# Performance work log

Measured on AMD Instinct MI355X. Metric: run time of the kernel, lower is better.

Reference implementation:

```python
import jax, jax.numpy as jnp
import numpy as np

N = 65536      # nodes
E = 262144     # edges per metapath
K = 8          # sampled edges per node
NMP = 2        # metapaths (n_mp)
DEPTH = 2      # layers
H = 4          # heads
D = 256        # prep_len / hidden (= H*PH)
PH = 64        # per-head output dim
ED = 64        # raw edge embedding dim


def setup_inputs() -> dict:
    key = jax.random.key(0)
    ks = jax.random.split(key, 16)
    s = 1.0 / np.sqrt(D)
    return {
        "feats": jax.random.normal(ks[0], (N, D), jnp.float32),
        "edge_emb": jax.random.normal(ks[1], (NMP, E, ED), jnp.float32),
        "edge_node_adj": jax.random.randint(ks[2], (NMP, E, 2), 0, N, dtype=jnp.int32),
        "node2edge_idx": jax.random.randint(ks[3], (NMP, N, K), 0, E, dtype=jnp.int32),
        "W_prep0": jax.random.normal(ks[4], (D, D), jnp.float32) * s,
        "W_prep1": jax.random.normal(ks[5], (D, D), jnp.float32) * s,
        "W_eprep": jax.random.normal(ks[6], (NMP, ED, D), jnp.float32) * (1.0 / np.sqrt(ED)),
        "a_e": jax.random.normal(ks[7], (NMP, DEPTH, H, D), jnp.float32) * s,
        "a_n": jax.random.normal(ks[8], (NMP, DEPTH, H, D), jnp.float32) * s,
        "W_e": jax.random.normal(ks[9], (NMP, DEPTH, H, D, PH), jnp.float32) * s,
        "a_s": jax.random.normal(ks[10], (NMP, DEPTH, H, D), jnp.float32) * s,
        "a_edge": jax.random.normal(ks[11], (NMP, DEPTH, H, D), jnp.float32) * s,
        "W_self": jax.random.normal(ks[12], (NMP, DEPTH, H, D, PH), jnp.float32) * s,
        "W_nb": jax.random.normal(ks[13], (NMP, DEPTH, H, D, PH), jnp.float32) * s,
    }


def _forward(feats, edge_emb, edge_node_adj, node2edge_idx,
             W_prep0, W_prep1, W_eprep, a_e, a_n, W_e, a_s, a_edge, W_self, W_nb):
    dummy = feats @ W_prep0     # prep(layer_idx=0)  [N,D]
    base = feats @ W_prep1      # prep(layer_idx=1)  [N,D]
    outputs = []
    for mp in range(NMP):
        x = base
        edges = edge_emb[mp] @ W_eprep[mp]           # [E,D]
        ena = edge_node_adj[mp]                      # [E,2]
        n2e = node2edge_idx[mp]                      # [N,K]
        skips = []
        for L in range(DEPTH):
            # --- edge aggregator: gather 2 endpoint node feats, attend, project ---
            ep = x[ena]                              # [E,2,D] gather
            s_e = jax.nn.leaky_relu(
                jnp.einsum('eqd,hd->ehq', ep, a_n[mp, L])
                + jnp.einsum('ed,hd->eh', edges, a_e[mp, L])[..., None], 0.2)  # [E,H,2]
            alp = jax.nn.softmax(s_e, axis=-1)
            agg = jnp.einsum('ehq,eqd->ehd', alp, ep)                          # [E,H,D]
            e_out = jax.nn.elu(
                jnp.einsum('ehd,hdp->ehp', edges[:, None, :] + agg, W_e[mp, L])
            ).reshape(E, H * PH)                                               # [E,D]
            # --- node aggregator: gather K sampled edge feats (OLD edges), attend ---
            xin = x if L > 0 else dummy              # layer 0 self-feature uses dummy prep
            eg = edges[n2e]                          # [N,K,D] gather
            s_n = jax.nn.leaky_relu(
                jnp.einsum('nd,hd->nh', xin, a_s[mp, L])[:, :, None]
                + jnp.einsum('nkd,hd->nhk', eg, a_edge[mp, L]), 0.2)           # [N,H,K]
            aln = jax.nn.softmax(s_n, axis=-1)
            nag = jnp.einsum('nhk,nkd->nhd', aln, eg)                          # [N,H,D]
            n_out = jax.nn.elu(
                jnp.einsum('nd,hdp->nhp', xin, W_self[mp, L])
                + jnp.einsum('nhd,hdp->nhp', nag, W_nb[mp, L])
            ).reshape(N, H * PH)                                               # [N,D]
            skips.append(n_out)
            x = n_out
            edges = e_out
        outputs.append(jnp.concatenate(skips, axis=-1))   # [N, DEPTH*D]
    return jnp.stack(outputs, axis=0)                     # [NMP, N, DEPTH*D]


def reference(feats, edge_emb, edge_node_adj, node2edge_idx,
              W_prep0, W_prep1, W_eprep, a_e, a_n, W_e, a_s, a_edge, W_self, W_nb):
    return _forward(feats, edge_emb, edge_node_adj, node2edge_idx,
                    W_prep0, W_prep1, W_eprep, a_e, a_n, W_e, a_s, a_edge, W_self, W_nb)
```

## Files before the change

kernel.cpp:

```cpp
#include <hip/hip_runtime.h>

typedef unsigned short ushort_t;
typedef unsigned int uint_t;

#define N_NODES 65536
#define N_EDGES 262144

typedef __attribute__((ext_vector_type(8))) short bf16x8;
typedef __attribute__((ext_vector_type(4))) float f32x4;

__device__ __forceinline__ ushort_t f2b(float x) {
  uint_t u = __float_as_uint(x);
  u += 0x7fffu + ((u >> 16) & 1u);
  return (ushort_t)(u >> 16);
}
__device__ __forceinline__ void dec8(uint4 v, float* f) {
  f[0] = __uint_as_float(v.x << 16); f[1] = __uint_as_float(v.x & 0xffff0000u);
  f[2] = __uint_as_float(v.y << 16); f[3] = __uint_as_float(v.y & 0xffff0000u);
  f[4] = __uint_as_float(v.z << 16); f[5] = __uint_as_float(v.z & 0xffff0000u);
  f[6] = __uint_as_float(v.w << 16); f[7] = __uint_as_float(v.w & 0xffff0000u);
}
__device__ __forceinline__ void dec4(uint2 v, float* f) {
  f[0] = __uint_as_float(v.x << 16); f[1] = __uint_as_float(v.x & 0xffff0000u);
  f[2] = __uint_as_float(v.y << 16); f[3] = __uint_as_float(v.y & 0xffff0000u);
}
__device__ __forceinline__ uint4 enc8(const float* f) {
  uint4 v;
  v.x = (uint_t)f2b(f[0]) | ((uint_t)f2b(f[1]) << 16);
  v.y = (uint_t)f2b(f[2]) | ((uint_t)f2b(f[3]) << 16);
  v.z = (uint_t)f2b(f[4]) | ((uint_t)f2b(f[5]) << 16);
  v.w = (uint_t)f2b(f[6]) | ((uint_t)f2b(f[7]) << 16);
  return v;
}
__device__ __forceinline__ uint2 enc4(const float* f) {
  uint2 v;
  v.x = (uint_t)f2b(f[0]) | ((uint_t)f2b(f[1]) << 16);
  v.y = (uint_t)f2b(f[2]) | ((uint_t)f2b(f[3]) << 16);
  return v;
}
__device__ __forceinline__ void ld8(const float* p, float* f) {
  float4 v0 = *(const float4*)p;
  float4 v1 = *(const float4*)(p + 4);
  f[0]=v0.x; f[1]=v0.y; f[2]=v0.z; f[3]=v0.w;
  f[4]=v1.x; f[5]=v1.y; f[6]=v1.z; f[7]=v1.w;
}

#define ELUF(v) ((v) > 0.f ? (v) : __expf(v) - 1.f)

__device__ __forceinline__ void async16(void* lds, const void* g) {
  __builtin_amdgcn_global_load_lds(
      (const __attribute__((address_space(1))) void*)g,
      (__attribute__((address_space(3))) void*)lds, 16, 0, 0);
}

__global__ void wt_kernel(const float* __restrict__ src, ushort_t* __restrict__ dst,
                          int K, int N) {
  long m = blockIdx.y;
  long base = m * (long)K * N;
  int tid = blockIdx.x * 256 + threadIdx.x;
  if (tid >= K * N) return;
  int k = tid % K, n = tid / K;
  dst[base + (long)n * K + k] = f2b(src[base + (long)k * N + n]);
}

__global__ __launch_bounds__(256, 2) void gemm_mfma(
    const float* __restrict__ A, const ushort_t* __restrict__ Wt,
    ushort_t* __restrict__ outb, int K) {
  __shared__ __align__(16) char smem[4096 + 16384];
  ushort_t (*sA)[32] = (ushort_t(*)[32])smem;
  ushort_t (*sB)[32] = (ushort_t(*)[32])(smem + 4096);
  int t = threadIdx.x, w = t >> 6, l = t & 63;
  long r0 = (long)blockIdx.x * 64;
  f32x4 zero = {0.f, 0.f, 0.f, 0.f};
  f32x4 acc[4][4];
#pragma unroll
  for (int mt = 0; mt < 4; ++mt)
#pragma unroll
    for (int nt = 0; nt < 4; ++nt) acc[mt][nt] = zero;

  for (int kc = 0; kc < K / 32; ++kc) {
    __syncthreads();
    {
      int r = t >> 2, ks8 = (t & 3) * 8;
      float f[8]; ld8(A + (r0 + r) * (long)K + kc * 32 + ks8, f);
      *(uint4*)&sA[r][ks8] = enc8(f);
    }
#pragma unroll
    for (int j = 0; j < 4; ++j) {
      int u = (w * 4 + j) * 64 + l;
      int n = u >> 2, ks = u & 3;
      async16((char*)sB + (w * 4 + j) * 1024, Wt + (long)n * K + kc * 32 + ks * 8);
    }
    __syncthreads();
    bf16x8 af[4], bf[4];
#pragma unroll
    for (int mt = 0; mt < 4; ++mt)
      af[mt] = *(const bf16x8*)&sA[mt * 16 + (l & 15)][(l >> 4) * 8];
#pragma unroll
    for (int nt = 0; nt < 4; ++nt)
      bf[nt] = *(const bf16x8*)&sB[w * 64 + nt * 16 + (l & 15)][(l >> 4) * 8];
#pragma unroll
    for (int mt = 0; mt < 4; ++mt)
#pragma unroll
      for (int nt = 0; nt < 4; ++nt)
        acc[mt][nt] = __builtin_amdgcn_mfma_f32_16x16x32_bf16(af[mt], bf[nt], acc[mt][nt], 0, 0, 0);
  }
#pragma unroll
  for (int mt = 0; mt < 4; ++mt)
#pragma unroll
    for (int nt = 0; nt < 4; ++nt)
#pragma unroll
      for (int i = 0; i < 4; ++i) {
        long row = r0 + mt * 16 + (l >> 4) * 4 + i;
        int col = w * 64 + nt * 16 + (l & 15);
        outb[row * 256 + col] = f2b(acc[mt][nt][i]);
      }
}

__global__ __launch_bounds__(256, 2) void gemm_eproj(
    const ushort_t* __restrict__ A, const ushort_t* __restrict__ Wt,
    const float* __restrict__ a_edge,
    ushort_t* __restrict__ outb, float* __restrict__ sed) {
  __shared__ __align__(16) char smem[4096 + 16384 + 8192];
  ushort_t (*sA)[32]   = (ushort_t(*)[32])smem;
  ushort_t (*sB)[32]   = (ushort_t(*)[32])(smem + 4096);
  ushort_t (*sAe)[256] = (ushort_t(*)[256])(smem + 20480);
  int t = threadIdx.x, w = t >> 6, l = t & 63;
  long r0 = (long)blockIdx.x * 64;

  {
    int row = t >> 4, seg = (t & 15) * 16;
    float f[16];
    if (row < 4) {
      ld8(a_edge + row * 256 + seg, f);
      ld8(a_edge + row * 256 + seg + 8, f + 8);
    } else {
#pragma unroll
      for (int i = 0; i < 16; ++i) f[i] = 0.f;
    }
    *(uint4*)&sAe[row][seg] = enc8(f);
    *(uint4*)&sAe[row][seg + 8] = enc8(f + 8);
  }

  f32x4 zero = {0.f, 0.f, 0.f, 0.f};
  f32x4 acc[4][4];
  f32x4 accs[4];
#pragma unroll
  for (int mt = 0; mt < 4; ++mt) {
    accs[mt] = zero;
#pragma unroll
    for (int nt = 0; nt < 4; ++nt) acc[mt][nt] = zero;
  }

  for (int kc = 0; kc < 8; ++kc) {
    __syncthreads();
    async16((char*)sA + w * 1024, A + (r0 + (t >> 2)) * 256 + kc * 32 + (t & 3) * 8);
#pragma unroll
    for (int j = 0; j < 4; ++j) {
      int u = (w * 4 + j) * 64 + l;
      int n = u >> 2, ks = u & 3;
      async16((char*)sB + (w * 4 + j) * 1024, Wt + (long)n * 256 + kc * 32 + ks * 8);
    }
    __syncthreads();
    bf16x8 af[4], bf[4];
#pragma unroll
    for (int mt = 0; mt < 4; ++mt)
      af[mt] = *(const bf16x8*)&sA[mt * 16 + (l & 15)][(l >> 4) * 8];
#pragma unroll
    for (int nt = 0; nt < 4; ++nt)
      bf[nt] = *(const bf16x8*)&sB[w * 64 + nt * 16 + (l & 15)][(l >> 4) * 8];
#pragma unroll
    for (int mt = 0; mt < 4; ++mt)
#pragma unroll
      for (int nt = 0; nt < 4; ++nt)
        acc[mt][nt] = __builtin_amdgcn_mfma_f32_16x16x32_bf16(af[mt], bf[nt], acc[mt][nt], 0, 0, 0);
    if (w == 0) {
      bf16x8 bs = *(const bf16x8*)&sAe[l & 15][kc * 32 + (l >> 4) * 8];
#pragma unroll
      for (int mt = 0; mt < 4; ++mt)
        accs[mt] = __builtin_amdgcn_mfma_f32_16x16x32_bf16(af[mt], bs, accs[mt], 0, 0, 0);
    }
  }
#pragma unroll
  for (int mt = 0; mt < 4; ++mt)
#pragma unroll
    for (int nt = 0; nt < 4; ++nt)
#pragma unroll
      for (int i = 0; i < 4; ++i) {
        long row = r0 + mt * 16 + (l >> 4) * 4 + i;
        int col = w * 64 + nt * 16 + (l & 15);
        outb[row * 256 + col] = f2b(acc[mt][nt][i]);
      }
  if (w == 0 && (l & 15) < 4) {
#pragma unroll
    for (int mt = 0; mt < 4; ++mt)
#pragma unroll
      for (int i = 0; i < 4; ++i) {
        long row = r0 + mt * 16 + (l >> 4) * 4 + i;
        sed[row * 4 + (l & 15)] = accs[mt][i];
      }
  }
}

__global__ __launch_bounds__(256, 2) void edge_kernel(
    const ushort_t* __restrict__ xb,
    const ushort_t* __restrict__ ein,
    ushort_t* __restrict__ eout,
    const int* __restrict__ ena,
    const float* __restrict__ a_n, const float* __restrict__ a_e,
    const ushort_t* __restrict__ Wt) {
  __shared__ __align__(16) char smem[8192 + 16384 + 4096 + 1024 + 256 + 16];
  ushort_t (*sY)[32][32] = (ushort_t(*)[32][32])smem;
  ushort_t (*sB)[32]     = (ushort_t(*)[32])(smem + 8192);
  ushort_t (*sAf)[256]   = (ushort_t(*)[256])(smem + 24576);
  float    (*sAlp)[4][2] = (float(*)[4][2])(smem + 28672);
  int* sIdx              = (int*)(smem + 29696);
  ushort_t* sOut         = (ushort_t*)smem;

  int t = threadIdx.x, w = t >> 6, l = t & 63;
  long e0 = (long)blockIdx.x * 32;

  if (t < 64) sIdx[(t & 1) * 32 + (t >> 1)] = ena[(e0 + (t >> 1)) * 2 + (t & 1)];
  {
    int row = t >> 5, dof = (t & 31) * 8;
    const float* src = (row < 4 ? a_n + row * 256 : a_e + (row - 4) * 256) + dof;
    float f[8]; ld8(src, f);
    *(uint4*)&sAf[row][dof] = enc8(f);
  }
  __syncthreads();

  int eT = t >> 3, sT = t & 7;
  int nid0 = sIdx[eT], nid1 = sIdx[32 + eT];
  const ushort_t* pxe = ein + (e0 + eT) * 256;
  const ushort_t* px0 = xb + (long)nid0 * 256;
  const ushort_t* px1 = xb + (long)nid1 * 256;

  float an0[4] = {0,0,0,0}, an1[4] = {0,0,0,0}, aee[4] = {0,0,0,0};
#pragma unroll
  for (int kc = 0; kc < 8; ++kc) {
    int dof = kc * 32 + sT * 4;
    float xe[4], x0[4], x1[4];
    dec4(*(const uint2*)(pxe + dof), xe);
    dec4(*(const uint2*)(px0 + dof), x0);
    dec4(*(const uint2*)(px1 + dof), x1);
#pragma unroll
    for (int h = 0; h < 4; ++h) {
      float av[4], bv[4];
      dec4(*(const uint2*)&sAf[h][dof], av);
      dec4(*(const uint2*)&sAf[4 + h][dof], bv);
#pragma unroll
      for (int d = 0; d < 4; ++d) {
        an0[h] += x0[d] * av[d];
        an1[h] += x1[d] * av[d];
        aee[h] += xe[d] * bv[d];
      }
    }
  }
#pragma unroll
  for (int m = 1; m <= 4; m <<= 1)
#pragma unroll
    for (int h = 0; h < 4; ++h) {
      an0[h] += __shfl_xor(an0[h], m, 64);
      an1[h] += __shfl_xor(an1[h], m, 64);
      aee[h] += __shfl_xor(aee[h], m, 64);
    }
  if (sT == 0) {
#pragma unroll
    for (int h = 0; h < 4; ++h) {
      float s0 = an0[h] + aee[h]; s0 = s0 > 0.f ? s0 : 0.2f * s0;
      float s1 = an1[h] + aee[h]; s1 = s1 > 0.f ? s1 : 0.2f * s1;
      float mx = fmaxf(s0, s1);
      float g0 = __expf(s0 - mx), g1 = __expf(s1 - mx);
      float inv = 1.f / (g0 + g1);
      sAlp[eT][h][0] = g0 * inv;
      sAlp[eT][h][1] = g1 * inv;
    }
  }
  __syncthreads();
  float alp[4][2];
#pragma unroll
  for (int h = 0; h < 4; ++h) {
    alp[h][0] = sAlp[eT][h][0];
    alp[h][1] = sAlp[eT][h][1];
  }

  f32x4 zero = {0.f, 0.f, 0.f, 0.f};
  f32x4 acc[2][4];
#pragma unroll
  for (int mt = 0; mt < 2; ++mt)
#pragma unroll
    for (int nt = 0; nt < 4; ++nt) acc[mt][nt] = zero;

  int ks4 = sT * 4;
  for (int kc = 0; kc < 8; ++kc) {
    __syncthreads();
#pragma unroll
    for (int j = 0; j < 4; ++j) {
      int u = (w * 4 + j) * 64 + l;
      int n = u >> 2, ks = u & 3;
      async16((char*)sB + (w * 4 + j) * 1024, Wt + (long)n * 256 + kc * 32 + ks * 8);
    }
    {
      int dof = kc * 32 + ks4;
      float xe[4], x0[4], x1[4];
      dec4(*(const uint2*)(pxe + dof), xe);
      dec4(*(const uint2*)(px0 + dof), x0);
      dec4(*(const uint2*)(px1 + dof), x1);
#pragma unroll
      for (int h = 0; h < 4; ++h) {
        float y[4];
#pragma unroll
        for (int d = 0; d < 4; ++d)
          y[d] = xe[d] + alp[h][0] * x0[d] + alp[h][1] * x1[d];
        *(uint2*)&sY[h][eT][ks4] = enc4(y);
      }
    }
    __syncthreads();
    bf16x8 af[2], bf[4];
#pragma unroll
    for (int mt = 0; mt < 2; ++mt)
      af[mt] = *(const bf16x8*)&sY[w][mt * 16 + (l & 15)][(l >> 4) * 8];
#pragma unroll
    for (int nt = 0; nt < 4; ++nt)
      bf[nt] = *(const bf16x8*)&sB[w * 64 + nt * 16 + (l & 15)][(l >> 4) * 8];
#pragma unroll
    for (int mt = 0; mt < 2; ++mt)
#pragma unroll
      for (int nt = 0; nt < 4; ++nt)
        acc[mt][nt] = __builtin_amdgcn_mfma_f32_16x16x32_bf16(af[mt], bf[nt], acc[mt][nt], 0, 0, 0);
  }
  __syncthreads();
#pragma unroll
  for (int mt = 0; mt < 2; ++mt)
#pragma unroll
    for (int nt = 0; nt < 4; ++nt)
#pragma unroll
      for (int i = 0; i < 4; ++i) {
        int row = mt * 16 + (l >> 4) * 4 + i;
        int col = w * 64 + nt * 16 + (l & 15);
        sOut[row * 264 + col] = f2b(ELUF(acc[mt][nt][i]));
      }
  __syncthreads();
#pragma unroll
  for (int j = 0; j < 4; ++j) {
    int u = t + j * 256;
    int r = u >> 5, ks = u & 31;
    *(uint4*)(eout + (e0 + r) * 256 + ks * 8) = *(const uint4*)&sOut[r * 264 + ks * 8];
  }
}

__global__ __launch_bounds__(256, 2) void node_out(
    const ushort_t* __restrict__ xb,
    const int* __restrict__ n2e,
    const ushort_t* __restrict__ eproj,
    const float* __restrict__ sed,
    const float* __restrict__ a_s,
    const ushort_t* __restrict__ WtS,
    float* __restrict__ outp,
    ushort_t* __restrict__ xout) {
  __shared__ __align__(16) char smem[33280 + 1024 + 4096 + 4096];
  ushort_t (*sX)[32]   = (ushort_t(*)[32])smem;
  ushort_t (*sBs)[32]  = (ushort_t(*)[32])(smem + 2048);
  ushort_t (*sAs)[256] = (ushort_t(*)[256])(smem + 18432);
  float* sOutF         = (float*)smem;
  int*   sIdx          = (int*)(smem + 33280);
  float* sSe           = (float*)(smem + 34304);
  float* sAln          = (float*)(smem + 38400);
  int t = threadIdx.x, w = t >> 6, l = t & 63;
  long n0 = (long)blockIdx.x * 32;

  {
    int e = n2e[n0 * 8 + t];
    sIdx[t] = e;
    *(float4*)&sSe[t * 4] = *(const float4*)(sed + (long)e * 4);
  }
  if (t < 128) {
    int row = t >> 5, dof = (t & 31) * 8;
    float f[8]; ld8(a_s + row * 256 + dof, f);
    *(uint4*)&sAs[row][dof] = enc8(f);
  }

  f32x4 zero = {0.f, 0.f, 0.f, 0.f};
  f32x4 acc[2][4];
#pragma unroll
  for (int mt = 0; mt < 2; ++mt)
#pragma unroll
    for (int nt = 0; nt < 4; ++nt) acc[mt][nt] = zero;
  float ssp = 0.f;
  int sn = t >> 3, shalf = (t & 1) * 16, sh = (t >> 1) & 3;

  for (int kc = 0; kc < 8; ++kc) {
    __syncthreads();
    if (w == 0) {
#pragma unroll
      for (int j = 0; j < 2; ++j) {
        int u = j * 64 + l;
        int r = u >> 2, ks = u & 3;
        async16((char*)sX + j * 1024, xb + (n0 + r) * 256 + kc * 32 + ks * 8);
      }
    }
#pragma unroll
    for (int j = 0; j < 4; ++j) {
      int u = (w * 4 + j) * 64 + l;
      int n = u >> 2, ks = u & 3;
      async16((char*)sBs + (w * 4 + j) * 1024, WtS + (long)n * 256 + kc * 32 + ks * 8);
    }
    __syncthreads();
    bf16x8 ax[2], bs[4];
#pragma unroll
    for (int mt = 0; mt < 2; ++mt)
      ax[mt] = *(const bf16x8*)&sX[mt * 16 + (l & 15)][(l >> 4) * 8];
#pragma unroll
    for (int nt = 0; nt < 4; ++nt)
      bs[nt] = *(const bf16x8*)&sBs[w * 64 + nt * 16 + (l & 15)][(l >> 4) * 8];
#pragma unroll
    for (int mt = 0; mt < 2; ++mt)
#pragma unroll
      for (int nt = 0; nt < 4; ++nt)
        acc[mt][nt] = __builtin_amdgcn_mfma_f32_16x16x32_bf16(ax[mt], bs[nt], acc[mt][nt], 0, 0, 0);
    {
      float xv[16], av[16];
      dec8(*(const uint4*)&sX[sn][shalf], xv);
      dec8(*(const uint4*)&sX[sn][shalf + 8], xv + 8);
      dec8(*(const uint4*)&sAs[sh][kc * 32 + shalf], av);
      dec8(*(const uint4*)&sAs[sh][kc * 32 + shalf + 8], av + 8);
#pragma unroll
      for (int d = 0; d < 16; ++d) ssp += xv[d] * av[d];
    }
  }
  __syncthreads();
#pragma unroll
  for (int mt = 0; mt < 2; ++mt)
#pragma unroll
    for (int nt = 0; nt < 4; ++nt)
#pragma unroll
      for (int i = 0; i < 4; ++i) {
        int row = mt * 16 + (l >> 4) * 4 + i;
        int col = w * 64 + nt * 16 + (l & 15);
        sOutF[row * 260 + col] = acc[mt][nt][i];
      }
  float ssv = ssp + __shfl_xor(ssp, 1, 64);
  if (!(t & 1)) {
    float sv[8], mx = -1e30f;
#pragma unroll
    for (int k = 0; k < 8; ++k) {
      float s = ssv + sSe[(sn * 8 + k) * 4 + sh];
      s = s > 0.f ? s : 0.2f * s;
      sv[k] = s; mx = fmaxf(mx, s);
    }
    float sum = 0.f;
#pragma unroll
    for (int k = 0; k < 8; ++k) { sv[k] = __expf(sv[k] - mx); sum += sv[k]; }
    float inv = 1.f / sum;
#pragma unroll
    for (int k = 0; k < 8; ++k) sAln[(sn * 4 + sh) * 8 + k] = sv[k] * inv;
  }
  __syncthreads();

  int nT = t >> 3, sT = t & 7, hh = sT >> 1, dof = sT * 32;
  float wts[8];
#pragma unroll
  for (int k = 0; k < 8; ++k) wts[k] = sAln[(nT * 4 + hh) * 8 + k];
  int eidx[8];
#pragma unroll
  for (int k = 0; k < 8; ++k) eidx[k] = sIdx[nT * 8 + k];
  float o[32];
#pragma unroll
  for (int j = 0; j < 8; ++j) {
    float4 sv = *(const float4*)&sOutF[nT * 260 + dof + j * 4];
    o[j * 4 + 0] = sv.x; o[j * 4 + 1] = sv.y; o[j * 4 + 2] = sv.z; o[j * 4 + 3] = sv.w;
  }
#pragma unroll
  for (int k = 0; k < 8; ++k) {
    const ushort_t* pr = eproj + (long)eidx[k] * 256 + dof;
    float v[32];
    dec8(*(const uint4*)(pr),      v);
    dec8(*(const uint4*)(pr + 8),  v + 8);
    dec8(*(const uint4*)(pr + 16), v + 16);
    dec8(*(const uint4*)(pr + 24), v + 24);
    float wk = wts[k];
#pragma unroll
    for (int d = 0; d < 32; ++d) o[d] += wk * v[d];
  }
  long row = n0 + nT;
  float res[32];
#pragma unroll
  for (int d = 0; d < 32; ++d) res[d] = ELUF(o[d]);
  float* po = outp + row * 512 + dof;
#pragma unroll
  for (int j = 0; j < 8; ++j) {
    float4 q;
    q.x = res[j * 4 + 0]; q.y = res[j * 4 + 1]; q.z = res[j * 4 + 2]; q.w = res[j * 4 + 3];
    *(float4*)(po + j * 4) = q;
  }
  if (xout) {
#pragma unroll
    for (int j = 0; j < 4; ++j)
      *(uint4*)(xout + row * 256 + dof + j * 8) = enc8(res + j * 8);
  }
}

extern "C" void kernel_launch(void* const* d_in, const int* in_sizes, int n_in,
                              void* d_out, int out_size, void* d_ws, size_t ws_size,
                              hipStream_t stream) {
  (void)in_sizes; (void)n_in; (void)out_size; (void)ws_size;
  const float* feats  = (const float*)d_in[0];
  const float* eemb   = (const float*)d_in[1];
  const int*   adj    = (const int*)d_in[2];
  const int*   n2e    = (const int*)d_in[3];
  const float* Wp0    = (const float*)d_in[4];
  const float* Wp1    = (const float*)d_in[5];
  const float* Wep    = (const float*)d_in[6];
  const float* a_e    = (const float*)d_in[7];
  const float* a_n    = (const float*)d_in[8];
  const float* W_e    = (const float*)d_in[9];
  const float* a_s    = (const float*)d_in[10];
  const float* a_edge = (const float*)d_in[11];
  const float* W_self = (const float*)d_in[12];
  const float* W_nb   = (const float*)d_in[13];
  float* out = (float*)d_out;

  char* w = (char*)d_ws;
  ushort_t* dummy_bf = (ushort_t*)w; w += (size_t)N_NODES * 256 * 2;
  ushort_t* base_bf  = (ushort_t*)w; w += (size_t)N_NODES * 256 * 2;
  ushort_t* edgesA   = (ushort_t*)w; w += (size_t)N_EDGES * 256 * 2;
  ushort_t* edgesB   = (ushort_t*)w; w += (size_t)N_EDGES * 256 * 2;
  ushort_t* eproj    = (ushort_t*)w; w += (size_t)N_EDGES * 256 * 2;
  float*    sed      = (float*)w;    w += (size_t)N_EDGES * 4 * 4;
  ushort_t* xl1      = (ushort_t*)w; w += (size_t)N_NODES * 256 * 2;
  ushort_t* WtP0     = (ushort_t*)w; w += 256 * 256 * 2;
  ushort_t* WtP1     = (ushort_t*)w; w += 256 * 256 * 2;
  ushort_t* WtEp     = (ushort_t*)w; w += 2 * 256 * 64 * 2;
  ushort_t* WtE      = (ushort_t*)w; w += 16 * 16384 * 2;
  ushort_t* WtS      = (ushort_t*)w; w += 16 * 16384 * 2;
  ushort_t* WtN      = (ushort_t*)w; w += 16 * 16384 * 2;

  wt_kernel<<<dim3(256, 1), 256, 0, stream>>>(Wp0, WtP0, 256, 256);
  wt_kernel<<<dim3(256, 1), 256, 0, stream>>>(Wp1, WtP1, 256, 256);
  wt_kernel<<<dim3(64, 2), 256, 0, stream>>>(Wep, WtEp, 64, 256);
  wt_kernel<<<dim3(64, 16), 256, 0, stream>>>(W_e, WtE, 256, 64);
  wt_kernel<<<dim3(64, 16), 256, 0, stream>>>(W_self, WtS, 256, 64);
  wt_kernel<<<dim3(64, 16), 256, 0, stream>>>(W_nb, WtN, 256, 64);

  gemm_mfma<<<N_NODES / 64, 256, 0, stream>>>(feats, WtP0, dummy_bf, 256);
  gemm_mfma<<<N_NODES / 64, 256, 0, stream>>>(feats, WtP1, base_bf, 256);

  for (int mp = 0; mp < 2; ++mp) {
    const int* adj_mp = adj + (size_t)mp * N_EDGES * 2;
    const int* n2e_mp = n2e + (size_t)mp * N_NODES * 8;
    size_t ao0 = (size_t)(mp * 2 + 0) * 1024, ao1 = (size_t)(mp * 2 + 1) * 1024;
    size_t wo0 = (size_t)(mp * 2 + 0) * 65536, wo1 = (size_t)(mp * 2 + 1) * 65536;

    gemm_mfma<<<N_EDGES / 64, 256, 0, stream>>>(
        eemb + (size_t)mp * N_EDGES * 64, WtEp + (size_t)mp * 16384, edgesA, 64);

    gemm_eproj<<<N_EDGES / 64, 256, 0, stream>>>(edgesA, WtN + wo0, a_edge + ao0, eproj, sed);
    edge_kernel<<<N_EDGES / 32, 256, 0, stream>>>(base_bf, edgesA, edgesB, adj_mp,
                                                  a_n + ao0, a_e + ao0, WtE + wo0);
    node_out<<<N_NODES / 32, 256, 0, stream>>>(dummy_bf, n2e_mp, eproj, sed,
                                               a_s + ao0, WtS + wo0,
                                               out + (size_t)mp * N_NODES * 512, xl1);
    gemm_eproj<<<N_EDGES / 64, 256, 0, stream>>>(edgesB, WtN + wo1, a_edge + ao1, eproj, sed);
    node_out<<<N_NODES / 32, 256, 0, stream>>>(xl1, n2e_mp, eproj, sed,
                                               a_s + ao1, WtS + wo1,
                                               out + (size_t)mp * N_NODES * 512 + 256,
                                               (ushort_t*)nullptr);
  }
}
```

Baseline: 1.589 ms.

## Project edges and nodes through W_e before gather and fuse next-layer projection

The edge aggregator now uses linearity. Edge embeddings and node features are projected through W_e separately, and the per-head attention scores come out of the same MFMA GEMMs. A new edge_combine kernel gathers the projected endpoint rows, mixes them with the attention weights and applies ELU. It then immediately multiplies the result by the next layer's W_nb, so the intermediate edge tensor is never materialized and the separate second gemm_eproj launch disappears. In exchange there is an extra node-sized GEMM, buffers are aliased across stages, and rounding is slightly different because the projection now happens before the mix.

```diff
diff --git a/kernel.cpp b/kernel.cpp
--- a/kernel.cpp
+++ b/kernel.cpp
@@ -119,14 +119,107 @@
 
 __global__ __launch_bounds__(256, 2) void gemm_eproj(
     const ushort_t* __restrict__ A, const ushort_t* __restrict__ Wt,
-    const float* __restrict__ a_edge,
-    ushort_t* __restrict__ outb, float* __restrict__ sed) {
+    const float* __restrict__ a_vec,
+    ushort_t* __restrict__ outb, float* __restrict__ sco) {
   __shared__ __align__(16) char smem[4096 + 16384 + 8192];
   ushort_t (*sA)[32]   = (ushort_t(*)[32])smem;
   ushort_t (*sB)[32]   = (ushort_t(*)[32])(smem + 4096);
   ushort_t (*sAe)[256] = (ushort_t(*)[256])(smem + 20480);
   int t = threadIdx.x, w = t >> 6, l = t & 63;
   long r0 = (long)blockIdx.x * 64;
+
+  {
+    int row = t >> 4, seg = (t & 15) * 16;
+    float f[16];
+    if (row < 4) {
+      ld8(a_vec + row * 256 + seg, f);
+      ld8(a_vec + row * 256 + seg + 8, f + 8);
+    } else {
+#pragma unroll
+      for (int i = 0; i < 16; ++i) f[i] = 0.f;
+    }
+    *(uint4*)&sAe[row][seg] = enc8(f);
+    *(uint4*)&sAe[row][seg + 8] = enc8(f + 8);
+  }
+
+  f32x4 zero = {0.f, 0.f, 0.f, 0.f};
+  f32x4 acc[4][4];
+  f32x4 accs[4];
+#pragma unroll
+  for (int mt = 0; mt < 4; ++mt) {
+    accs[mt] = zero;
+#pragma unroll
+    for (int nt = 0; nt < 4; ++nt) acc[mt][nt] = zero;
+  }
+
+  for (int kc = 0; kc < 8; ++kc) {
+    __syncthreads();
+    async16((char*)sA + w * 1024, A + (r0 + (t >> 2)) * 256 + kc * 32 + (t & 3) * 8);
+#pragma unroll
+    for (int j = 0; j < 4; ++j) {
+      int u = (w * 4 + j) * 64 + l;
+      int n = u >> 2, ks = u & 3;
+      async16((char*)sB + (w * 4 + j) * 1024, Wt + (long)n * 256 + kc * 32 + ks * 8);
+    }
+    __syncthreads();
+    bf16x8 af[4], bf[4];
+#pragma unroll
+    for (int mt = 0; mt < 4; ++mt)
+      af[mt] = *(const bf16x8*)&sA[mt * 16 + (l & 15)][(l >> 4) * 8];
+#pragma unroll
+    for (int nt = 0; nt < 4; ++nt)
+      bf[nt] = *(const bf16x8*)&sB[w * 64 + nt * 16 + (l & 15)][(l >> 4) * 8];
+#pragma unroll
+    for (int mt = 0; mt < 4; ++mt)
+#pragma unroll
+      for (int nt = 0; nt < 4; ++nt)
+        acc[mt][nt] = __builtin_amdgcn_mfma_f32_16x16x32_bf16(af[mt], bf[nt], acc[mt][nt], 0, 0, 0);
+    if (w == 0) {
+      bf16x8 bs = *(const bf16x8*)&sAe[l & 15][kc * 32 + (l >> 4) * 8];
+#pragma unroll
+      for (int mt = 0; mt < 4; ++mt)
+        accs[mt] = __builtin_amdgcn_mfma_f32_16x16x32_bf16(af[mt], bs, accs[mt], 0, 0, 0);
+    }
+  }
+#pragma unroll
+  for (int mt = 0; mt < 4; ++mt)
+#pragma unroll
+    for (int nt = 0; nt < 4; ++nt)
+#pragma unroll
+      for (int i = 0; i < 4; ++i) {
+        long row = r0 + mt * 16 + (l >> 4) * 4 + i;
+        int col = w * 64 + nt * 16 + (l & 15);
+        outb[row * 256 + col] = f2b(acc[mt][nt][i]);
+      }
+  if (w == 0 && (l & 15) < 4) {
+#pragma unroll
+    for (int mt = 0; mt < 4; ++mt)
+#pragma unroll
+      for (int i = 0; i < 4; ++i) {
+        long row = r0 + mt * 16 + (l >> 4) * 4 + i;
+        sco[row * 4 + (l & 15)] = accs[mt][i];
+      }
+  }
+}
+
+__global__ __launch_bounds__(256, 2) void edge_combine(
+    const int* __restrict__ ena,
+    const ushort_t* __restrict__ eprojE,
+    const ushort_t* __restrict__ xprojE,
+    const float* __restrict__ xan,
+    const float* __restrict__ sea,
+    const ushort_t* __restrict__ Wt,
+    const float* __restrict__ a_edge,
+    ushort_t* __restrict__ outb,
+    float* __restrict__ sed) {
+  __shared__ __align__(16) char smem[4096 + 16384 + 8192 + 2048 + 512];
+  ushort_t (*sY)[32]   = (ushort_t(*)[32])smem;
+  ushort_t (*sB)[32]   = (ushort_t(*)[32])(smem + 4096);
+  ushort_t (*sAe)[256] = (ushort_t(*)[256])(smem + 20480);
+  float (*sAlp)[4][2]  = (float(*)[4][2])(smem + 28672);
+  int* sIdx            = (int*)(smem + 30720);
+  int t = threadIdx.x, w = t >> 6, l = t & 63;
+  long e0 = (long)blockIdx.x * 64;
 
   {
     int row = t >> 4, seg = (t & 15) * 16;
@@ -141,6 +234,27 @@
     *(uint4*)&sAe[row][seg] = enc8(f);
     *(uint4*)&sAe[row][seg + 8] = enc8(f + 8);
   }
+  if (t < 128) sIdx[t] = ena[e0 * 2 + t];
+  __syncthreads();
+
+  {
+    int e = t >> 2, h = t & 3;
+    int n0 = sIdx[2 * e], n1 = sIdx[2 * e + 1];
+    float sE = sea[(e0 + e) * 4 + h];
+    float s0 = xan[(long)n0 * 4 + h] + sE; s0 = s0 > 0.f ? s0 : 0.2f * s0;
+    float s1 = xan[(long)n1 * 4 + h] + sE; s1 = s1 > 0.f ? s1 : 0.2f * s1;
+    float mx = fmaxf(s0, s1);
+    float g0 = __expf(s0 - mx), g1 = __expf(s1 - mx);
+    float inv = 1.f / (g0 + g1);
+    sAlp[e][h][0] = g0 * inv;
+    sAlp[e][h][1] = g1 * inv;
+  }
+
+  int r = t >> 2, c0 = (t & 3) * 8;
+  int n0r = sIdx[2 * r], n1r = sIdx[2 * r + 1];
+  const ushort_t* pe = eprojE + (e0 + r) * 256 + c0;
+  const ushort_t* p0 = xprojE + (long)n0r * 256 + c0;
+  const ushort_t* p1 = xprojE + (long)n1r * 256 + c0;
 
   f32x4 zero = {0.f, 0.f, 0.f, 0.f};
   f32x4 acc[4][4];
@@ -154,18 +268,31 @@
 
   for (int kc = 0; kc < 8; ++kc) {
     __syncthreads();
-    async16((char*)sA + w * 1024, A + (r0 + (t >> 2)) * 256 + kc * 32 + (t & 3) * 8);
 #pragma unroll
     for (int j = 0; j < 4; ++j) {
       int u = (w * 4 + j) * 64 + l;
       int n = u >> 2, ks = u & 3;
       async16((char*)sB + (w * 4 + j) * 1024, Wt + (long)n * 256 + kc * 32 + ks * 8);
     }
+    {
+      int h = kc >> 1;
+      float a0 = sAlp[r][h][0], a1 = sAlp[r][h][1];
+      float ep[8], x0[8], x1[8], y[8];
+      dec8(*(const uint4*)(pe + kc * 32), ep);
+      dec8(*(const uint4*)(p0 + kc * 32), x0);
+      dec8(*(const uint4*)(p1 + kc * 32), x1);
+#pragma unroll
+      for (int d = 0; d < 8; ++d) {
+        float v = ep[d] + a0 * x0[d] + a1 * x1[d];
+        y[d] = ELUF(v);
+      }
+      *(uint4*)&sY[r][c0] = enc8(y);
+    }
     __syncthreads();
     bf16x8 af[4], bf[4];
 #pragma unroll
     for (int mt = 0; mt < 4; ++mt)
-      af[mt] = *(const bf16x8*)&sA[mt * 16 + (l & 15)][(l >> 4) * 8];
+      af[mt] = *(const bf16x8*)&sY[mt * 16 + (l & 15)][(l >> 4) * 8];
 #pragma unroll
     for (int nt = 0; nt < 4; ++nt)
       bf[nt] = *(const bf16x8*)&sB[w * 64 + nt * 16 + (l & 15)][(l >> 4) * 8];
@@ -187,7 +314,7 @@
     for (int nt = 0; nt < 4; ++nt)
 #pragma unroll
       for (int i = 0; i < 4; ++i) {
-        long row = r0 + mt * 16 + (l >> 4) * 4 + i;
+        long row = e0 + mt * 16 + (l >> 4) * 4 + i;
         int col = w * 64 + nt * 16 + (l & 15);
         outb[row * 256 + col] = f2b(acc[mt][nt][i]);
       }
@@ -196,156 +323,9 @@
     for (int mt = 0; mt < 4; ++mt)
 #pragma unroll
       for (int i = 0; i < 4; ++i) {
-        long row = r0 + mt * 16 + (l >> 4) * 4 + i;
+        long row = e0 + mt * 16 + (l >> 4) * 4 + i;
         sed[row * 4 + (l & 15)] = accs[mt][i];
       }
-  }
-}
-
-__global__ __launch_bounds__(256, 2) void edge_kernel(
-    const ushort_t* __restrict__ xb,
-    const ushort_t* __restrict__ ein,
-    ushort_t* __restrict__ eout,
-    const int* __restrict__ ena,
-    const float* __restrict__ a_n, const float* __restrict__ a_e,
-    const ushort_t* __restrict__ Wt) {
-  __shared__ __align__(16) char smem[8192 + 16384 + 4096 + 1024 + 256 + 16];
-  ushort_t (*sY)[32][32] = (ushort_t(*)[32][32])smem;
-  ushort_t (*sB)[32]     = (ushort_t(*)[32])(smem + 8192);
-  ushort_t (*sAf)[256]   = (ushort_t(*)[256])(smem + 24576);
-  float    (*sAlp)[4][2] = (float(*)[4][2])(smem + 28672);
-  int* sIdx              = (int*)(smem + 29696);
-  ushort_t* sOut         = (ushort_t*)smem;
-
-  int t = threadIdx.x, w = t >> 6, l = t & 63;
-  long e0 = (long)blockIdx.x * 32;
-
-  if (t < 64) sIdx[(t & 1) * 32 + (t >> 1)] = ena[(e0 + (t >> 1)) * 2 + (t & 1)];
-  {
-    int row = t >> 5, dof = (t & 31) * 8;
-    const float* src = (row < 4 ? a_n + row * 256 : a_e + (row - 4) * 256) + dof;
-    float f[8]; ld8(src, f);
-    *(uint4*)&sAf[row][dof] = enc8(f);
-  }
-  __syncthreads();
-
-  int eT = t >> 3, sT = t & 7;
-  int nid0 = sIdx[eT], nid1 = sIdx[32 + eT];
-  const ushort_t* pxe = ein + (e0 + eT) * 256;
-  const ushort_t* px0 = xb + (long)nid0 * 256;
-  const ushort_t* px1 = xb + (long)nid1 * 256;
-
-  float an0[4] = {0,0,0,0}, an1[4] = {0,0,0,0}, aee[4] = {0,0,0,0};
-#pragma unroll
-  for (int kc = 0; kc < 8; ++kc) {
-    int dof = kc * 32 + sT * 4;
-    float xe[4], x0[4], x1[4];
-    dec4(*(const uint2*)(pxe + dof), xe);
-    dec4(*(const uint2*)(px0 + dof), x0);
-    dec4(*(const uint2*)(px1 + dof), x1);
-#pragma unroll
-    for (int h = 0; h < 4; ++h) {
-      float av[4], bv[4];
-      dec4(*(const uint2*)&sAf[h][dof], av);
-      dec4(*(const uint2*)&sAf[4 + h][dof], bv);
-#pragma unroll
-      for (int d = 0; d < 4; ++d) {
-        an0[h] += x0[d] * av[d];
-        an1[h] += x1[d] * av[d];
-        aee[h] += xe[d] * bv[d];
-      }
-    }
-  }
-#pragma unroll
-  for (int m = 1; m <= 4; m <<= 1)
-#pragma unroll
-    for (int h = 0; h < 4; ++h) {
-      an0[h] += __shfl_xor(an0[h], m, 64);
-      an1[h] += __shfl_xor(an1[h], m, 64);
-      aee[h] += __shfl_xor(aee[h], m, 64);
-    }
-  if (sT == 0) {
-#pragma unroll
-    for (int h = 0; h < 4; ++h) {
-      float s0 = an0[h] + aee[h]; s0 = s0 > 0.f ? s0 : 0.2f * s0;
-      float s1 = an1[h] + aee[h]; s1 = s1 > 0.f ? s1 : 0.2f * s1;
-      float mx = fmaxf(s0, s1);
-      float g0 = __expf(s0 - mx), g1 = __expf(s1 - mx);
-      float inv = 1.f / (g0 + g1);
-      sAlp[eT][h][0] = g0 * inv;
-      sAlp[eT][h][1] = g1 * inv;
-    }
-  }
-  __syncthreads();
-  float alp[4][2];
-#pragma unroll
-  for (int h = 0; h < 4; ++h) {
-    alp[h][0] = sAlp[eT][h][0];
-    alp[h][1] = sAlp[eT][h][1];
-  }
-
-  f32x4 zero = {0.f, 0.f, 0.f, 0.f};
-  f32x4 acc[2][4];
-#pragma unroll
-  for (int mt = 0; mt < 2; ++mt)
-#pragma unroll
-    for (int nt = 0; nt < 4; ++nt) acc[mt][nt] = zero;
-
-  int ks4 = sT * 4;
-  for (int kc = 0; kc < 8; ++kc) {
-    __syncthreads();
-#pragma unroll
-    for (int j = 0; j < 4; ++j) {
-      int u = (w * 4 + j) * 64 + l;
-      int n = u >> 2, ks = u & 3;
-      async16((char*)sB + (w * 4 + j) * 1024, Wt + (long)n * 256 + kc * 32 + ks * 8);
-    }
-    {
-      int dof = kc * 32 + ks4;
-      float xe[4], x0[4], x1[4];
-      dec4(*(const uint2*)(pxe + dof), xe);
-      dec4(*(const uint2*)(px0 + dof), x0);
-      dec4(*(const uint2*)(px1 + dof), x1);
-#pragma unroll
-      for (int h = 0; h < 4; ++h) {
-        float y[4];
-#pragma unroll
-        for (int d = 0; d < 4; ++d)
-          y[d] = xe[d] + alp[h][0] * x0[d] + alp[h][1] * x1[d];
-        *(uint2*)&sY[h][eT][ks4] = enc4(y);
-      }
-    }
-    __syncthreads();
-    bf16x8 af[2], bf[4];
-#pragma unroll
-    for (int mt = 0; mt < 2; ++mt)
-      af[mt] = *(const bf16x8*)&sY[w][mt * 16 + (l & 15)][(l >> 4) * 8];
-#pragma unroll
-    for (int nt = 0; nt < 4; ++nt)
-      bf[nt] = *(const bf16x8*)&sB[w * 64 + nt * 16 + (l & 15)][(l >> 4) * 8];
-#pragma unroll
-    for (int mt = 0; mt < 2; ++mt)
-#pragma unroll
-      for (int nt = 0; nt < 4; ++nt)
-        acc[mt][nt] = __builtin_amdgcn_mfma_f32_16x16x32_bf16(af[mt], bf[nt], acc[mt][nt], 0, 0, 0);
-  }
-  __syncthreads();
-#pragma unroll
-  for (int mt = 0; mt < 2; ++mt)
-#pragma unroll
-    for (int nt = 0; nt < 4; ++nt)
-#pragma unroll
-      for (int i = 0; i < 4; ++i) {
-        int row = mt * 16 + (l >> 4) * 4 + i;
-        int col = w * 64 + nt * 16 + (l & 15);
-        sOut[row * 264 + col] = f2b(ELUF(acc[mt][nt][i]));
-      }
-  __syncthreads();
-#pragma unroll
-  for (int j = 0; j < 4; ++j) {
-    int u = t + j * 256;
-    int r = u >> 5, ks = u & 31;
-    *(uint4*)(eout + (e0 + r) * 256 + ks * 8) = *(const uint4*)&sOut[r * 264 + ks * 8];
   }
 }
 
@@ -523,11 +503,14 @@
   char* w = (char*)d_ws;
   ushort_t* dummy_bf = (ushort_t*)w; w += (size_t)N_NODES * 256 * 2;
   ushort_t* base_bf  = (ushort_t*)w; w += (size_t)N_NODES * 256 * 2;
-  ushort_t* edgesA   = (ushort_t*)w; w += (size_t)N_EDGES * 256 * 2;
-  ushort_t* edgesB   = (ushort_t*)w; w += (size_t)N_EDGES * 256 * 2;
-  ushort_t* eproj    = (ushort_t*)w; w += (size_t)N_EDGES * 256 * 2;
-  float*    sed      = (float*)w;    w += (size_t)N_EDGES * 4 * 4;
-  ushort_t* xl1      = (ushort_t*)w; w += (size_t)N_NODES * 256 * 2;
+  ushort_t* bufEA    = (ushort_t*)w; w += (size_t)N_EDGES * 256 * 2;
+  ushort_t* bufEB    = (ushort_t*)w; w += (size_t)N_EDGES * 256 * 2;
+  ushort_t* bufEC    = (ushort_t*)w; w += (size_t)N_EDGES * 256 * 2;
+  ushort_t* bufX     = (ushort_t*)w; w += (size_t)N_NODES * 256 * 2;
+  float*    sea      = (float*)w;    w += (size_t)N_EDGES * 4 * 4;
+  float*    sed0     = (float*)w;    w += (size_t)N_EDGES * 4 * 4;
+  float*    sed1     = (float*)w;    w += (size_t)N_EDGES * 4 * 4;
+  float*    xan      = (float*)w;    w += (size_t)N_NODES * 4 * 4;
   ushort_t* WtP0     = (ushort_t*)w; w += 256 * 256 * 2;
   ushort_t* WtP1     = (ushort_t*)w; w += 256 * 256 * 2;
   ushort_t* WtEp     = (ushort_t*)w; w += 2 * 256 * 64 * 2;
@@ -551,17 +534,24 @@
     size_t ao0 = (size_t)(mp * 2 + 0) * 1024, ao1 = (size_t)(mp * 2 + 1) * 1024;
     size_t wo0 = (size_t)(mp * 2 + 0) * 65536, wo1 = (size_t)(mp * 2 + 1) * 65536;
 
+    ushort_t* edgesA  = bufEA;
+    ushort_t* eprojE  = bufEB;
+    ushort_t* eproj0  = bufEC;
+    ushort_t* eprojL1 = bufEA;
+    ushort_t* xprojE  = bufX;
+    ushort_t* xl1     = bufX;
+
     gemm_mfma<<<N_EDGES / 64, 256, 0, stream>>>(
         eemb + (size_t)mp * N_EDGES * 64, WtEp + (size_t)mp * 16384, edgesA, 64);
-
-    gemm_eproj<<<N_EDGES / 64, 256, 0, stream>>>(edgesA, WtN + wo0, a_edge + ao0, eproj, sed);
-    edge_kernel<<<N_EDGES / 32, 256, 0, stream>>>(base_bf, edgesA, edgesB, adj_mp,
-                                                  a_n + ao0, a_e + ao0, WtE + wo0);
-    node_out<<<N_NODES / 32, 256, 0, stream>>>(dummy_bf, n2e_mp, eproj, sed,
+    gemm_eproj<<<N_EDGES / 64, 256, 0, stream>>>(edgesA, WtE + wo0, a_e + ao0, eprojE, sea);
+    gemm_eproj<<<N_NODES / 64, 256, 0, stream>>>(base_bf, WtE + wo0, a_n + ao0, xprojE, xan);
+    gemm_eproj<<<N_EDGES / 64, 256, 0, stream>>>(edgesA, WtN + wo0, a_edge + ao0, eproj0, sed0);
+    edge_combine<<<N_EDGES / 64, 256, 0, stream>>>(adj_mp, eprojE, xprojE, xan, sea,
+                                                   WtN + wo1, a_edge + ao1, eprojL1, sed1);
+    node_out<<<N_NODES / 32, 256, 0, stream>>>(dummy_bf, n2e_mp, eproj0, sed0,
                                                a_s + ao0, WtS + wo0,
                                                out + (size_t)mp * N_NODES * 512, xl1);
-    gemm_eproj<<<N_EDGES / 64, 256, 0, stream>>>(edgesB, WtN + wo1, a_edge + ao1, eproj, sed);
-    node_out<<<N_NODES / 32, 256, 0, stream>>>(xl1, n2e_mp, eproj, sed,
+    node_out<<<N_NODES / 32, 256, 0, stream>>>(xl1, n2e_mp, eprojL1, sed1,
                                                a_s + ao1, WtS + wo1,
                                                out + (size_t)mp * N_NODES * 512 + 256,
                                                (ushort_t*)nullptr);
```

After: 1.584 ms. No clear change (-0.3%).
